# Optimization experiments

Hardware: AMD Instinct MI355X
Metric: run time of the kernel (lower is better)

Reference implementation:

```python
import jax, jax.numpy as jnp
import numpy as np

USER_VOCAB = 1_000_000
MOVIE_VOCAB = 100_000
EMB_DIM = 64
BATCH = 65536
H1, H2 = 256, 128  # over_arch_layer_sizes


def setup_inputs() -> dict:
    key = jax.random.key(0)
    ks = jax.random.split(key, 10)
    inv = 1.0 / np.sqrt(EMB_DIM)
    return {
        "user_ids": jax.random.randint(ks[0], (BATCH,), 0, USER_VOCAB),
        "movie_ids": jax.random.randint(ks[1], (BATCH,), 0, MOVIE_VOCAB),
        "emb_user": jax.random.normal(ks[2], (USER_VOCAB, EMB_DIM), jnp.float32) * inv,
        "emb_movie": jax.random.normal(ks[3], (MOVIE_VOCAB, EMB_DIM), jnp.float32) * inv,
        "W1": jax.random.normal(ks[4], (EMB_DIM, H1), jnp.float32) * (1.0 / np.sqrt(EMB_DIM)),
        "b1": jnp.zeros((H1,), jnp.float32),
        "W2": jax.random.normal(ks[5], (H1, H2), jnp.float32) * (1.0 / np.sqrt(H1)),
        "b2": jnp.zeros((H2,), jnp.float32),
        "W3": jax.random.normal(ks[6], (H2, 1), jnp.float32) * (1.0 / np.sqrt(H2)),
        "b3": jnp.zeros((1,), jnp.float32),
    }


def reference(user_ids, movie_ids, emb_user, emb_movie, W1, b1, W2, b2, W3, b3):
    B = user_ids.shape[0]
    # sparse gather per feature (hotness = 1)
    eu = emb_user[user_ids]    # [B, D]
    em = emb_movie[movie_ids]  # [B, D]
    # concat jagged outputs along rows, matching torch.cat(..., dim=0)
    x = jnp.concatenate([eu, em], axis=0)  # [2B, D]
    h = jax.nn.relu(x @ W1 + b1)
    h = jax.nn.relu(h @ W2 + b2)
    p = h @ W3 + b3                        # [2B, 1]
    # view(num_features, batch).t().sum(-1) -> sum over features per sample
    return p.reshape(2, B).sum(axis=0)     # [B]
```

## Files before the change

kernel.cpp:

```cpp
#include <hip/hip_runtime.h>


typedef __attribute__((ext_vector_type(8))) short bf16x8;
typedef __attribute__((ext_vector_type(4))) float f32x4;

__device__ __forceinline__ unsigned int bfr(float f) {
  unsigned int u = __builtin_bit_cast(unsigned int, f);
  return (u + 0x7fffu + ((u >> 16) & 1u)) >> 16;
}
__device__ __forceinline__ unsigned int bfrh(float f) {
  unsigned int u = __builtin_bit_cast(unsigned int, f);
  return (u + 0x7fffu + ((u >> 16) & 1u)) & 0xffff0000u;
}
__device__ __forceinline__ unsigned int pk2(float lo, float hi) {
  return bfr(lo) | bfrh(hi);
}

__global__ __launch_bounds__(512, 2) void movielens_mlp(
    const int* __restrict__ uids, const int* __restrict__ mids,
    const float* __restrict__ EU, const float* __restrict__ EM,
    const float* __restrict__ W1, const float* __restrict__ B1,
    const float* __restrict__ W2, const float* __restrict__ B2,
    const float* __restrict__ W3, const float* __restrict__ B3,
    float* __restrict__ out) {
  __shared__ __align__(16) unsigned short w1f[16 * 2 * 512];
  __shared__ __align__(16) unsigned short w2f[8 * 8 * 512];
  __shared__ __align__(16) unsigned short h1f[8 * 4 * 512];

  const int tid = threadIdx.x;

  {
    const int u = tid & 63;
#pragma unroll
    for (int pass = 0; pass < 2; ++pass) {
      const int qd = (tid >> 6) + 8 * pass;
      const float* src = W1 + (qd * 4) * 256 + 4 * u;
      const float4 r0 = *(const float4*)(src);
      const float4 r1 = *(const float4*)(src + 256);
      const float4 r2 = *(const float4*)(src + 512);
      const float4 r3 = *(const float4*)(src + 768);
      const float c0[4] = {r0.x, r0.y, r0.z, r0.w};
      const float c1[4] = {r1.x, r1.y, r1.z, r1.w};
      const float c2[4] = {r2.x, r2.y, r2.z, r2.w};
      const float c3[4] = {r3.x, r3.y, r3.z, r3.w};
      const int kt = qd >> 3, g = (qd >> 1) & 3, bo = (qd & 1) * 4;
#pragma unroll
      for (int p = 0; p < 4; ++p) {
        const int n = 4 * u + p, nt = n >> 4, mm = n & 15;
        uint2 pk;
        pk.x = pk2(c0[p], c1[p]);
        pk.y = pk2(c2[p], c3[p]);
        *(uint2*)&w1f[(nt * 2 + kt) * 512 + (g * 16 + mm) * 8 + bo] = pk;
      }
    }
    const int u2 = tid & 31;
#pragma unroll
    for (int pass = 0; pass < 4; ++pass) {
      const int qd = (tid >> 5) + 16 * pass;
      const float* src = W2 + (qd * 4) * 128 + 4 * u2;
      const float4 r0 = *(const float4*)(src);
      const float4 r1 = *(const float4*)(src + 128);
      const float4 r2 = *(const float4*)(src + 256);
      const float4 r3 = *(const float4*)(src + 384);
      const float c0[4] = {r0.x, r0.y, r0.z, r0.w};
      const float c1[4] = {r1.x, r1.y, r1.z, r1.w};
      const float c2[4] = {r2.x, r2.y, r2.z, r2.w};
      const float c3[4] = {r3.x, r3.y, r3.z, r3.w};
      const int hq = qd >> 3, g = (qd >> 1) & 3, bo = (qd & 1) * 4;
#pragma unroll
      for (int p = 0; p < 4; ++p) {
        const int n = 4 * u2 + p, nt2 = n >> 4, mm = n & 15;
        uint2 pk;
        pk.x = pk2(c0[p], c1[p]);
        pk.y = pk2(c2[p], c3[p]);
        *(uint2*)&w2f[(nt2 * 8 + hq) * 512 + (g * 16 + mm) * 8 + bo] = pk;
      }
    }
  }
  __syncthreads();

  const int lane = tid & 63;
  const int wv = tid >> 6;
  const int m = lane & 15;
  const int g = lane >> 4;
  unsigned short* __restrict__ h1 = &h1f[wv * 4 * 512];

  const int sbase = blockIdx.x * 256 + wv * 32;
  const int su = sbase + m, sv = su + 16;

  const float* rp[4];
  rp[0] = EU + (size_t)uids[su] * 64;
  rp[1] = EU + (size_t)uids[sv] * 64;
  rp[2] = EM + (size_t)mids[su] * 64;
  rp[3] = EM + (size_t)mids[sv] * 64;

  bf16x8 xf[4][2];
#pragma unroll
  for (int mt = 0; mt < 4; ++mt) {
#pragma unroll
    for (int kt = 0; kt < 2; ++kt) {
      const float4 a = *(const float4*)(rp[mt] + kt * 32 + 8 * g);
      const float4 b = *(const float4*)(rp[mt] + kt * 32 + 8 * g + 4);
      uint4 t;
      t.x = pk2(a.x, a.y);
      t.y = pk2(a.z, a.w);
      t.z = pk2(b.x, b.y);
      t.w = pk2(b.z, b.w);
      xf[mt][kt] = __builtin_bit_cast(bf16x8, t);
    }
  }

  f32x4 acc2[4][8];
#pragma unroll
  for (int nt2 = 0; nt2 < 8; ++nt2) {
    const float4 bv = *(const float4*)(B2 + nt2 * 16 + 4 * g);
#pragma unroll
    for (int mt = 0; mt < 4; ++mt) {
      acc2[mt][nt2][0] = bv.x; acc2[mt][nt2][1] = bv.y;
      acc2[mt][nt2][2] = bv.z; acc2[mt][nt2][3] = bv.w;
    }
  }

#pragma unroll 2
  for (int hq = 0; hq < 8; ++hq) {
#pragma unroll
    for (int ntloc = 0; ntloc < 2; ++ntloc) {
      const int fb = (hq * 4 + ntloc * 2) * 512;
      const bf16x8 wa0 = *(const bf16x8*)&w1f[fb + lane * 8];
      const bf16x8 wa1 = *(const bf16x8*)&w1f[fb + 512 + lane * 8];
      const float4 b1v = *(const float4*)(B1 + hq * 32 + ntloc * 16 + 4 * g);
      const int slot = (2 * ntloc + (g >> 1)) * 16 + m;
      const int wo = slot * 8 + (g & 1) * 4;
#pragma unroll
      for (int mt = 0; mt < 4; ++mt) {
        f32x4 acc;
        acc[0] = b1v.x; acc[1] = b1v.y; acc[2] = b1v.z; acc[3] = b1v.w;
        acc = __builtin_amdgcn_mfma_f32_16x16x32_bf16(wa0, xf[mt][0], acc, 0, 0, 0);
        acc = __builtin_amdgcn_mfma_f32_16x16x32_bf16(wa1, xf[mt][1], acc, 0, 0, 0);
        uint2 pk;
        pk.x = pk2(fmaxf(acc[0], 0.f), fmaxf(acc[1], 0.f));
        pk.y = pk2(fmaxf(acc[2], 0.f), fmaxf(acc[3], 0.f));
        *(uint2*)&h1[mt * 512 + wo] = pk;
      }
    }
    bf16x8 hf[4];
#pragma unroll
    for (int mt = 0; mt < 4; ++mt)
      hf[mt] = *(const bf16x8*)&h1[mt * 512 + lane * 8];
#pragma unroll
    for (int nt2 = 0; nt2 < 8; ++nt2) {
      const bf16x8 w2v = *(const bf16x8*)&w2f[(nt2 * 8 + hq) * 512 + lane * 8];
#pragma unroll
      for (int mt = 0; mt < 4; ++mt)
        acc2[mt][nt2] = __builtin_amdgcn_mfma_f32_16x16x32_bf16(w2v, hf[mt], acc2[mt][nt2], 0, 0, 0);
    }
  }

  const float b3v = B3[0];
  float part[4] = {0.f, 0.f, 0.f, 0.f};
#pragma unroll
  for (int nt2 = 0; nt2 < 8; ++nt2) {
    const float4 w3v = *(const float4*)(W3 + nt2 * 16 + 4 * g);
#pragma unroll
    for (int mt = 0; mt < 4; ++mt) {
      const f32x4 c = acc2[mt][nt2];
      part[mt] += fmaxf(c[0], 0.f) * w3v.x + fmaxf(c[1], 0.f) * w3v.y +
                  fmaxf(c[2], 0.f) * w3v.z + fmaxf(c[3], 0.f) * w3v.w;
    }
  }
#pragma unroll
  for (int mt = 0; mt < 4; ++mt) {
    part[mt] += __shfl_xor(part[mt], 16, 64);
    part[mt] += __shfl_xor(part[mt], 32, 64);
  }
  if (lane < 16) {
    out[sbase + lane] = part[0] + part[2] + 2.f * b3v;
  } else if (lane < 32) {
    out[sbase + lane] = part[1] + part[3] + 2.f * b3v;
  }
}

extern "C" void kernel_launch(void* const* d_in, const int* in_sizes, int n_in,
                              void* d_out, int out_size, void* d_ws, size_t ws_size,
                              hipStream_t stream) {
  const int* uids = (const int*)d_in[0];
  const int* mids = (const int*)d_in[1];
  const float* EU = (const float*)d_in[2];
  const float* EM = (const float*)d_in[3];
  const float* W1 = (const float*)d_in[4];
  const float* B1 = (const float*)d_in[5];
  const float* W2 = (const float*)d_in[6];
  const float* B2 = (const float*)d_in[7];
  const float* W3 = (const float*)d_in[8];
  const float* B3 = (const float*)d_in[9];
  float* out = (float*)d_out;

  const int B = in_sizes[0];
  const int nblk = B / 256;
  hipLaunchKernelGGL(movielens_mlp, dim3(nblk), dim3(512), 0, stream,
                     uids, mids, EU, EM, W1, B1, W2, B2, W3, B3, out);
}
```

Baseline: 25.95 us.

## Prepack W2 in a prep kernel, double-buffer h1 and prefetch embeddings early

A separate prep kernel now converts W2 to bf16 in MFMA fragment layout in workspace once per call. The main kernel reads it from global/L2 instead of staging it in LDS per block. Blocks shrink to 256 threads covering 128 samples, which frees LDS and raises the block count. Embedding gathers are issued before the W1 staging so their latency overlaps it. The layer-1 output is double-buffered so producing the next chunk overlaps the layer-2 MFMAs, at the cost of an extra kernel launch and W2 being re-fetched from cache by every wave.

```diff
diff --git a/kernel.cpp b/kernel.cpp
--- a/kernel.cpp
+++ b/kernel.cpp
@@ -16,24 +16,57 @@
   return bfr(lo) | bfrh(hi);
 }
 
-__global__ __launch_bounds__(512, 2) void movielens_mlp(
+__global__ __launch_bounds__(256) void prep_w2(const float* __restrict__ W2,
+                                               unsigned short* __restrict__ w2g) {
+  const int t = blockIdx.x * 256 + threadIdx.x;
+  const int fi = t >> 6, l = t & 63;
+  const int g = l >> 4, mm = l & 15;
+  const int nt2 = fi >> 3, hq = fi & 7;
+  const float* src = W2 + (hq * 32 + 8 * g) * 128 + nt2 * 16 + mm;
+  uint4 o;
+  o.x = pk2(src[0 * 128], src[1 * 128]);
+  o.y = pk2(src[2 * 128], src[3 * 128]);
+  o.z = pk2(src[4 * 128], src[5 * 128]);
+  o.w = pk2(src[6 * 128], src[7 * 128]);
+  *(uint4*)&w2g[fi * 512 + l * 8] = o;
+}
+
+__global__ __launch_bounds__(256, 2) void movielens_mlp(
     const int* __restrict__ uids, const int* __restrict__ mids,
     const float* __restrict__ EU, const float* __restrict__ EM,
     const float* __restrict__ W1, const float* __restrict__ B1,
-    const float* __restrict__ W2, const float* __restrict__ B2,
+    const unsigned short* __restrict__ w2g, const float* __restrict__ B2,
     const float* __restrict__ W3, const float* __restrict__ B3,
     float* __restrict__ out) {
   __shared__ __align__(16) unsigned short w1f[16 * 2 * 512];
-  __shared__ __align__(16) unsigned short w2f[8 * 8 * 512];
-  __shared__ __align__(16) unsigned short h1f[8 * 4 * 512];
+  __shared__ __align__(16) unsigned short h1f[4 * 2 * 4 * 512];
 
   const int tid = threadIdx.x;
+  const int lane = tid & 63, wv = tid >> 6;
+  const int m = lane & 15, g = lane >> 4;
+
+  const int sbase = blockIdx.x * 128 + wv * 32;
+  const int su = sbase + m, sv = su + 16;
+
+  const float* rp[4];
+  rp[0] = EU + (size_t)uids[su] * 64;
+  rp[1] = EU + (size_t)uids[sv] * 64;
+  rp[2] = EM + (size_t)mids[su] * 64;
+  rp[3] = EM + (size_t)mids[sv] * 64;
+  float4 xr[4][2][2];
+#pragma unroll
+  for (int mt = 0; mt < 4; ++mt)
+#pragma unroll
+    for (int kt = 0; kt < 2; ++kt) {
+      xr[mt][kt][0] = *(const float4*)(rp[mt] + kt * 32 + 8 * g);
+      xr[mt][kt][1] = *(const float4*)(rp[mt] + kt * 32 + 8 * g + 4);
+    }
 
   {
     const int u = tid & 63;
 #pragma unroll
-    for (int pass = 0; pass < 2; ++pass) {
-      const int qd = (tid >> 6) + 8 * pass;
+    for (int pass = 0; pass < 4; ++pass) {
+      const int qd = (tid >> 6) + 4 * pass;
       const float* src = W1 + (qd * 4) * 256 + 4 * u;
       const float4 r0 = *(const float4*)(src);
       const float4 r1 = *(const float4*)(src + 256);
@@ -43,64 +76,24 @@
       const float c1[4] = {r1.x, r1.y, r1.z, r1.w};
       const float c2[4] = {r2.x, r2.y, r2.z, r2.w};
       const float c3[4] = {r3.x, r3.y, r3.z, r3.w};
-      const int kt = qd >> 3, g = (qd >> 1) & 3, bo = (qd & 1) * 4;
+      const int kt = qd >> 3, gg = (qd >> 1) & 3, bo = (qd & 1) * 4;
 #pragma unroll
       for (int p = 0; p < 4; ++p) {
         const int n = 4 * u + p, nt = n >> 4, mm = n & 15;
         uint2 pk;
         pk.x = pk2(c0[p], c1[p]);
         pk.y = pk2(c2[p], c3[p]);
-        *(uint2*)&w1f[(nt * 2 + kt) * 512 + (g * 16 + mm) * 8 + bo] = pk;
+        *(uint2*)&w1f[(nt * 2 + kt) * 512 + (gg * 16 + mm) * 8 + bo] = pk;
       }
     }
-    const int u2 = tid & 31;
-#pragma unroll
-    for (int pass = 0; pass < 4; ++pass) {
-      const int qd = (tid >> 5) + 16 * pass;
-      const float* src = W2 + (qd * 4) * 128 + 4 * u2;
-      const float4 r0 = *(const float4*)(src);
-      const float4 r1 = *(const float4*)(src + 128);
-      const float4 r2 = *(const float4*)(src + 256);
-      const float4 r3 = *(const float4*)(src + 384);
-      const float c0[4] = {r0.x, r0.y, r0.z, r0.w};
-      const float c1[4] = {r1.x, r1.y, r1.z, r1.w};
-      const float c2[4] = {r2.x, r2.y, r2.z, r2.w};
-      const float c3[4] = {r3.x, r3.y, r3.z, r3.w};
-      const int hq = qd >> 3, g = (qd >> 1) & 3, bo = (qd & 1) * 4;
-#pragma unroll
-      for (int p = 0; p < 4; ++p) {
-        const int n = 4 * u2 + p, nt2 = n >> 4, mm = n & 15;
-        uint2 pk;
-        pk.x = pk2(c0[p], c1[p]);
-        pk.y = pk2(c2[p], c3[p]);
-        *(uint2*)&w2f[(nt2 * 8 + hq) * 512 + (g * 16 + mm) * 8 + bo] = pk;
-      }
-    }
-  }
-  __syncthreads();
-
-  const int lane = tid & 63;
-  const int wv = tid >> 6;
-  const int m = lane & 15;
-  const int g = lane >> 4;
-  unsigned short* __restrict__ h1 = &h1f[wv * 4 * 512];
-
-  const int sbase = blockIdx.x * 256 + wv * 32;
-  const int su = sbase + m, sv = su + 16;
-
-  const float* rp[4];
-  rp[0] = EU + (size_t)uids[su] * 64;
-  rp[1] = EU + (size_t)uids[sv] * 64;
-  rp[2] = EM + (size_t)mids[su] * 64;
-  rp[3] = EM + (size_t)mids[sv] * 64;
+  }
 
   bf16x8 xf[4][2];
 #pragma unroll
-  for (int mt = 0; mt < 4; ++mt) {
+  for (int mt = 0; mt < 4; ++mt)
 #pragma unroll
     for (int kt = 0; kt < 2; ++kt) {
-      const float4 a = *(const float4*)(rp[mt] + kt * 32 + 8 * g);
-      const float4 b = *(const float4*)(rp[mt] + kt * 32 + 8 * g + 4);
+      const float4 a = xr[mt][kt][0], b = xr[mt][kt][1];
       uint4 t;
       t.x = pk2(a.x, a.y);
       t.y = pk2(a.z, a.w);
@@ -108,29 +101,18 @@
       t.w = pk2(b.z, b.w);
       xf[mt][kt] = __builtin_bit_cast(bf16x8, t);
     }
-  }
-
-  f32x4 acc2[4][8];
-#pragma unroll
-  for (int nt2 = 0; nt2 < 8; ++nt2) {
-    const float4 bv = *(const float4*)(B2 + nt2 * 16 + 4 * g);
-#pragma unroll
-    for (int mt = 0; mt < 4; ++mt) {
-      acc2[mt][nt2][0] = bv.x; acc2[mt][nt2][1] = bv.y;
-      acc2[mt][nt2][2] = bv.z; acc2[mt][nt2][3] = bv.w;
-    }
-  }
-
-#pragma unroll 2
-  for (int hq = 0; hq < 8; ++hq) {
+  __syncthreads();
+
+  unsigned short* __restrict__ h1 = &h1f[wv * 4096];
+
+  auto produce = [&](int hq, unsigned short* buf) {
 #pragma unroll
     for (int ntloc = 0; ntloc < 2; ++ntloc) {
       const int fb = (hq * 4 + ntloc * 2) * 512;
       const bf16x8 wa0 = *(const bf16x8*)&w1f[fb + lane * 8];
       const bf16x8 wa1 = *(const bf16x8*)&w1f[fb + 512 + lane * 8];
       const float4 b1v = *(const float4*)(B1 + hq * 32 + ntloc * 16 + 4 * g);
-      const int slot = (2 * ntloc + (g >> 1)) * 16 + m;
-      const int wo = slot * 8 + (g & 1) * 4;
+      const int wo = ((2 * ntloc + (g >> 1)) * 16 + m) * 8 + (g & 1) * 4;
 #pragma unroll
       for (int mt = 0; mt < 4; ++mt) {
         f32x4 acc;
@@ -140,20 +122,42 @@
         uint2 pk;
         pk.x = pk2(fmaxf(acc[0], 0.f), fmaxf(acc[1], 0.f));
         pk.y = pk2(fmaxf(acc[2], 0.f), fmaxf(acc[3], 0.f));
-        *(uint2*)&h1[mt * 512 + wo] = pk;
+        *(uint2*)&buf[mt * 512 + wo] = pk;
       }
     }
+  };
+
+  f32x4 acc2[4][8];
+#pragma unroll
+  for (int nt2 = 0; nt2 < 8; ++nt2) {
+    const float4 bv = *(const float4*)(B2 + nt2 * 16 + 4 * g);
+#pragma unroll
+    for (int mt = 0; mt < 4; ++mt) {
+      acc2[mt][nt2][0] = bv.x; acc2[mt][nt2][1] = bv.y;
+      acc2[mt][nt2][2] = bv.z; acc2[mt][nt2][3] = bv.w;
+    }
+  }
+
+  produce(0, h1);
+
+#pragma unroll 2
+  for (int hq = 0; hq < 8; ++hq) {
+    bf16x8 w2v[8];
+#pragma unroll
+    for (int nt2 = 0; nt2 < 8; ++nt2)
+      w2v[nt2] = *(const bf16x8*)&w2g[(nt2 * 8 + hq) * 512 + lane * 8];
+    if (hq < 7) produce(hq + 1, h1 + ((hq + 1) & 1) * 2048);
+    unsigned short* cbuf = h1 + (hq & 1) * 2048;
     bf16x8 hf[4];
 #pragma unroll
     for (int mt = 0; mt < 4; ++mt)
-      hf[mt] = *(const bf16x8*)&h1[mt * 512 + lane * 8];
-#pragma unroll
-    for (int nt2 = 0; nt2 < 8; ++nt2) {
-      const bf16x8 w2v = *(const bf16x8*)&w2f[(nt2 * 8 + hq) * 512 + lane * 8];
+      hf[mt] = *(const bf16x8*)&cbuf[mt * 512 + lane * 8];
+#pragma unroll
+    for (int nt2 = 0; nt2 < 8; ++nt2)
 #pragma unroll
       for (int mt = 0; mt < 4; ++mt)
-        acc2[mt][nt2] = __builtin_amdgcn_mfma_f32_16x16x32_bf16(w2v, hf[mt], acc2[mt][nt2], 0, 0, 0);
-    }
+        acc2[mt][nt2] = __builtin_amdgcn_mfma_f32_16x16x32_bf16(
+            w2v[nt2], hf[mt], acc2[mt][nt2], 0, 0, 0);
   }
 
   const float b3v = B3[0];
@@ -194,9 +198,12 @@
   const float* W3 = (const float*)d_in[8];
   const float* B3 = (const float*)d_in[9];
   float* out = (float*)d_out;
+  unsigned short* w2g = (unsigned short*)d_ws;
+
+  hipLaunchKernelGGL(prep_w2, dim3(16), dim3(256), 0, stream, W2, w2g);
 
   const int B = in_sizes[0];
-  const int nblk = B / 256;
-  hipLaunchKernelGGL(movielens_mlp, dim3(nblk), dim3(512), 0, stream,
-                     uids, mids, EU, EM, W1, B1, W2, B2, W3, B3, out);
-}
+  const int nblk = B / 128;
+  hipLaunchKernelGGL(movielens_mlp, dim3(nblk), dim3(256), 0, stream,
+                     uids, mids, EU, EM, W1, B1, w2g, B2, W3, B3, out);
+}
```

New measurement: 29.05 us. 11.9% more time.

## Keep layer-1 activations in registers, use hardware bf16 convert, prefetch gathers early

Applied to the files above, without the earlier changes.

W1 rows are permuted in shared memory so the layer-1 MFMA output layout directly matches the B-operand layout of the layer-2 MFMA. This removes the per-wave h1 shared-memory round trip. The scalar bf16 rounding code is replaced with the v_cvt_pk_bf16_f32 instruction. The embedding gathers are issued before the weight staging and barrier, so their latency overlaps the LDS fill. The cost is higher register pressure from holding 32 float4 gather values across the weight-staging phase.

```diff
diff --git a/kernel.cpp b/kernel.cpp
--- a/kernel.cpp
+++ b/kernel.cpp
@@ -4,16 +4,10 @@
 typedef __attribute__((ext_vector_type(8))) short bf16x8;
 typedef __attribute__((ext_vector_type(4))) float f32x4;
 
-__device__ __forceinline__ unsigned int bfr(float f) {
-  unsigned int u = __builtin_bit_cast(unsigned int, f);
-  return (u + 0x7fffu + ((u >> 16) & 1u)) >> 16;
-}
-__device__ __forceinline__ unsigned int bfrh(float f) {
-  unsigned int u = __builtin_bit_cast(unsigned int, f);
-  return (u + 0x7fffu + ((u >> 16) & 1u)) & 0xffff0000u;
-}
-__device__ __forceinline__ unsigned int pk2(float lo, float hi) {
-  return bfr(lo) | bfrh(hi);
+__device__ __forceinline__ unsigned int cvt_pk(float lo, float hi) {
+  unsigned int r;
+  asm("v_cvt_pk_bf16_f32 %0, %1, %2" : "=v"(r) : "v"(lo), "v"(hi));
+  return r;
 }
 
 __global__ __launch_bounds__(512, 2) void movielens_mlp(
@@ -25,9 +19,27 @@
     float* __restrict__ out) {
   __shared__ __align__(16) unsigned short w1f[16 * 2 * 512];
   __shared__ __align__(16) unsigned short w2f[8 * 8 * 512];
-  __shared__ __align__(16) unsigned short h1f[8 * 4 * 512];
 
   const int tid = threadIdx.x;
+  const int lane = tid & 63, wv = tid >> 6;
+  const int m = lane & 15, g = lane >> 4;
+
+  const int sbase = blockIdx.x * 256 + wv * 32;
+  const int su = sbase + m, sv = su + 16;
+
+  const float* rp[4];
+  rp[0] = EU + (size_t)uids[su] * 64;
+  rp[1] = EU + (size_t)uids[sv] * 64;
+  rp[2] = EM + (size_t)mids[su] * 64;
+  rp[3] = EM + (size_t)mids[sv] * 64;
+  float4 xr[4][2][2];
+#pragma unroll
+  for (int mt = 0; mt < 4; ++mt)
+#pragma unroll
+    for (int kt = 0; kt < 2; ++kt) {
+      xr[mt][kt][0] = *(const float4*)(rp[mt] + kt * 32 + 8 * g);
+      xr[mt][kt][1] = *(const float4*)(rp[mt] + kt * 32 + 8 * g + 4);
+    }
 
   {
     const int u = tid & 63;
@@ -43,14 +55,17 @@
       const float c1[4] = {r1.x, r1.y, r1.z, r1.w};
       const float c2[4] = {r2.x, r2.y, r2.z, r2.w};
       const float c3[4] = {r3.x, r3.y, r3.z, r3.w};
-      const int kt = qd >> 3, g = (qd >> 1) & 3, bo = (qd & 1) * 4;
+      const int kt = qd >> 3, gg = (qd >> 1) & 3, bo = (qd & 1) * 4;
 #pragma unroll
       for (int p = 0; p < 4; ++p) {
-        const int n = 4 * u + p, nt = n >> 4, mm = n & 15;
+        const int n = 4 * u + p;
+        const int hq = n >> 5, cl = n & 31;
+        const int nt = (cl >> 2) & 1, mm = 4 * (cl >> 3) + (cl & 3);
+        const int fi = hq * 4 + nt * 2 + kt;
         uint2 pk;
-        pk.x = pk2(c0[p], c1[p]);
-        pk.y = pk2(c2[p], c3[p]);
-        *(uint2*)&w1f[(nt * 2 + kt) * 512 + (g * 16 + mm) * 8 + bo] = pk;
+        pk.x = cvt_pk(c0[p], c1[p]);
+        pk.y = cvt_pk(c2[p], c3[p]);
+        *(uint2*)&w1f[fi * 512 + (gg * 16 + mm) * 8 + bo] = pk;
       }
     }
     const int u2 = tid & 31;
@@ -66,49 +81,32 @@
       const float c1[4] = {r1.x, r1.y, r1.z, r1.w};
       const float c2[4] = {r2.x, r2.y, r2.z, r2.w};
       const float c3[4] = {r3.x, r3.y, r3.z, r3.w};
-      const int hq = qd >> 3, g = (qd >> 1) & 3, bo = (qd & 1) * 4;
+      const int hq2 = qd >> 3, gg = (qd >> 1) & 3, bo = (qd & 1) * 4;
 #pragma unroll
       for (int p = 0; p < 4; ++p) {
         const int n = 4 * u2 + p, nt2 = n >> 4, mm = n & 15;
         uint2 pk;
-        pk.x = pk2(c0[p], c1[p]);
-        pk.y = pk2(c2[p], c3[p]);
-        *(uint2*)&w2f[(nt2 * 8 + hq) * 512 + (g * 16 + mm) * 8 + bo] = pk;
+        pk.x = cvt_pk(c0[p], c1[p]);
+        pk.y = cvt_pk(c2[p], c3[p]);
+        *(uint2*)&w2f[(nt2 * 8 + hq2) * 512 + (gg * 16 + mm) * 8 + bo] = pk;
       }
     }
   }
-  __syncthreads();
-
-  const int lane = tid & 63;
-  const int wv = tid >> 6;
-  const int m = lane & 15;
-  const int g = lane >> 4;
-  unsigned short* __restrict__ h1 = &h1f[wv * 4 * 512];
-
-  const int sbase = blockIdx.x * 256 + wv * 32;
-  const int su = sbase + m, sv = su + 16;
-
-  const float* rp[4];
-  rp[0] = EU + (size_t)uids[su] * 64;
-  rp[1] = EU + (size_t)uids[sv] * 64;
-  rp[2] = EM + (size_t)mids[su] * 64;
-  rp[3] = EM + (size_t)mids[sv] * 64;
 
   bf16x8 xf[4][2];
 #pragma unroll
-  for (int mt = 0; mt < 4; ++mt) {
+  for (int mt = 0; mt < 4; ++mt)
 #pragma unroll
     for (int kt = 0; kt < 2; ++kt) {
-      const float4 a = *(const float4*)(rp[mt] + kt * 32 + 8 * g);
-      const float4 b = *(const float4*)(rp[mt] + kt * 32 + 8 * g + 4);
+      const float4 a = xr[mt][kt][0], b = xr[mt][kt][1];
       uint4 t;
-      t.x = pk2(a.x, a.y);
-      t.y = pk2(a.z, a.w);
-      t.z = pk2(b.x, b.y);
-      t.w = pk2(b.z, b.w);
+      t.x = cvt_pk(a.x, a.y);
+      t.y = cvt_pk(a.z, a.w);
+      t.z = cvt_pk(b.x, b.y);
+      t.w = cvt_pk(b.z, b.w);
       xf[mt][kt] = __builtin_bit_cast(bf16x8, t);
     }
-  }
+  __syncthreads();
 
   f32x4 acc2[4][8];
 #pragma unroll
@@ -123,36 +121,32 @@
 
 #pragma unroll 2
   for (int hq = 0; hq < 8; ++hq) {
+    uint4 hw[4];
 #pragma unroll
-    for (int ntloc = 0; ntloc < 2; ++ntloc) {
-      const int fb = (hq * 4 + ntloc * 2) * 512;
+    for (int nt = 0; nt < 2; ++nt) {
+      const int fb = (hq * 4 + nt * 2) * 512;
       const bf16x8 wa0 = *(const bf16x8*)&w1f[fb + lane * 8];
       const bf16x8 wa1 = *(const bf16x8*)&w1f[fb + 512 + lane * 8];
-      const float4 b1v = *(const float4*)(B1 + hq * 32 + ntloc * 16 + 4 * g);
-      const int slot = (2 * ntloc + (g >> 1)) * 16 + m;
-      const int wo = slot * 8 + (g & 1) * 4;
+      const float4 b1v = *(const float4*)(B1 + hq * 32 + 8 * g + 4 * nt);
 #pragma unroll
       for (int mt = 0; mt < 4; ++mt) {
         f32x4 acc;
         acc[0] = b1v.x; acc[1] = b1v.y; acc[2] = b1v.z; acc[3] = b1v.w;
         acc = __builtin_amdgcn_mfma_f32_16x16x32_bf16(wa0, xf[mt][0], acc, 0, 0, 0);
         acc = __builtin_amdgcn_mfma_f32_16x16x32_bf16(wa1, xf[mt][1], acc, 0, 0, 0);
-        uint2 pk;
-        pk.x = pk2(fmaxf(acc[0], 0.f), fmaxf(acc[1], 0.f));
-        pk.y = pk2(fmaxf(acc[2], 0.f), fmaxf(acc[3], 0.f));
-        *(uint2*)&h1[mt * 512 + wo] = pk;
+        const unsigned int wlo = cvt_pk(fmaxf(acc[0], 0.f), fmaxf(acc[1], 0.f));
+        const unsigned int whi = cvt_pk(fmaxf(acc[2], 0.f), fmaxf(acc[3], 0.f));
+        if (nt == 0) { hw[mt].x = wlo; hw[mt].y = whi; }
+        else         { hw[mt].z = wlo; hw[mt].w = whi; }
       }
     }
-    bf16x8 hf[4];
-#pragma unroll
-    for (int mt = 0; mt < 4; ++mt)
-      hf[mt] = *(const bf16x8*)&h1[mt * 512 + lane * 8];
 #pragma unroll
     for (int nt2 = 0; nt2 < 8; ++nt2) {
       const bf16x8 w2v = *(const bf16x8*)&w2f[(nt2 * 8 + hq) * 512 + lane * 8];
 #pragma unroll
       for (int mt = 0; mt < 4; ++mt)
-        acc2[mt][nt2] = __builtin_amdgcn_mfma_f32_16x16x32_bf16(w2v, hf[mt], acc2[mt][nt2], 0, 0, 0);
+        acc2[mt][nt2] = __builtin_amdgcn_mfma_f32_16x16x32_bf16(
+            w2v, __builtin_bit_cast(bf16x8, hw[mt]), acc2[mt][nt2], 0, 0, 0);
     }
   }
 
```

After: 22.25 us. -14.3%, faster.
